# Kernel optimization log

Hardware: AMD Instinct MI355X
Metric: run time of the kernel (lower is better)

Reference implementation:

```python
import jax, jax.numpy as jnp
import numpy as np

T = 10
EPS = 1e-05

def setup_inputs() -> dict:
    key = jax.random.key(0)
    k1, k2 = jax.random.split(key)
    B, C, H, W = 128, 64, 56, 56
    X = jax.random.normal(k1, (B, C, H, W), dtype=jnp.float32)
    beta = jnp.zeros((C,), dtype=jnp.float32)
    return {"X": X, "beta": beta}


def reference(X, beta):
    # Training-path of BWItnBlock.forward (grad enabled branch of iter_norm_batch)
    B, C, H, W = X.shape
    d = C                      # n_channels, num_groups g = 1
    m = B * H * W
    # x = X.transpose(0,1).view(g, d, -1)  -> [d, m] with g=1
    x = jnp.transpose(X, (1, 0, 2, 3)).reshape(d, m)
    mean = jnp.mean(x, axis=1, keepdims=True)          # [d, 1]
    xc = x - mean                                      # [d, m]
    I = jnp.eye(d, dtype=X.dtype)
    # Sigma = eps*I + xc xc^T / m
    Sigma = EPS * I + (xc @ xc.T) / m                  # [d, d]
    # fix_cov: multiply off-diagonal by 0.9, diagonal by 1.0
    fix = 0.9 + 0.1 * I
    Sigma = Sigma * fix
    rTr = 1.0 / jnp.trace(Sigma)                       # scalar (sum(Sigma * I))
    Sigma_N = Sigma * rTr
    # Newton-Schulz iterations for inverse sqrt: P <- 1.5 P - 0.5 P^3 Sigma_N
    P = I
    for _ in range(T):
        P = 1.5 * P - 0.5 * ((P @ P @ P) @ Sigma_N)
    wm = P * jnp.sqrt(rTr)                             # whitening matrix [d, d]
    xn = wm @ xc                                       # [d, m]
    X_hat = jnp.transpose(xn.reshape(C, B, H, W), (1, 0, 2, 3))
    X_hat = X_hat + beta.reshape(1, C, 1, 1)
    return X_hat
```

## Files before the change

### kernel.cpp

```cpp
#include <hip/hip_runtime.h>

#define CH 64
#define HW 3136
#define MTOT 401408
#define TPX 128
#define NBLK 784
#define TPB 4

typedef __attribute__((ext_vector_type(8))) short short8;
typedef __attribute__((ext_vector_type(4))) float f32x4;
typedef __attribute__((ext_vector_type(4))) unsigned int u32x4;

__device__ __forceinline__ void split8(const float4 a, const float4 b,
                                       short8& hi, short8& lo, float& ssum){
  const float f[8] = {a.x,a.y,a.z,a.w, b.x,b.y,b.z,b.w};
  u32x4 hp, lp;
#pragma unroll
  for (int j=0;j<4;++j){
    const unsigned int b0 = __float_as_uint(f[2*j]);
    const unsigned int b1 = __float_as_uint(f[2*j+1]);
    hp[j] = (b0 >> 16) | (b1 & 0xFFFF0000u);
    const float h0 = __uint_as_float(b0 & 0xFFFF0000u);
    const float h1 = __uint_as_float(b1 & 0xFFFF0000u);
    const unsigned int l0 = __float_as_uint(f[2*j]   - h0);
    const unsigned int l1 = __float_as_uint(f[2*j+1] - h1);
    lp[j] = (l0 >> 16) | (l1 & 0xFFFF0000u);
  }
  hi = __builtin_bit_cast(short8, hp);
  lo = __builtin_bit_cast(short8, lp);
  ssum += ((f[0]+f[1])+(f[2]+f[3])) + ((f[4]+f[5])+(f[6]+f[7]));
}

__global__ __launch_bounds__(256) void k1_cov(const float* __restrict__ X,
                                              float* __restrict__ SR){
  constexpr int RG[10] = {0,1,1,2,2,2,3,3,3,3};
  constexpr int CG[10] = {0,0,1,0,1,2,0,1,2,3};
  __shared__ __align__(16) float buf[2][64*TPX];
  __shared__ float chs[64];

  const int t   = threadIdx.x;
  const int wid = __builtin_amdgcn_readfirstlane(t >> 6);
  const int l   = t & 63;
  const int lr  = l & 15;
  const int q   = l >> 4;

  f32x4 acc[10];
#pragma unroll
  for (int bi=0; bi<10; ++bi) acc[bi] = (f32x4){0.f,0.f,0.f,0.f};
  float sums[4] = {0.f,0.f,0.f,0.f};

  auto stage = [&](int tl, float* dst){
    const unsigned mbase = (unsigned)(blockIdx.x*TPB + tl) * TPX;
#pragma unroll
    for (int j=0;j<8;++j){
      const int r  = 16*wid + 2*j + (l>>5);
      const int cb = (l&31) ^ (r&7);
      const unsigned m  = mbase + 4*cb;
      const unsigned b  = m / HW;
      const unsigned hw = m - b*HW;
      const float* src = X + (size_t)b*(CH*HW) + (size_t)r*HW + hw;
      __builtin_amdgcn_global_load_lds(
        (const __attribute__((address_space(1))) unsigned int*)src,
        (__attribute__((address_space(3))) unsigned int*)(dst + (16*wid + 2*j)*TPX),
        16, 0, 0);
    }
  };

  stage(0, buf[0]);
  int pb = 0;
#pragma unroll
  for (int tl=0; tl<TPB; ++tl){
    if (tl+1 < TPB){
      stage(tl+1, buf[pb^1]);
      asm volatile("s_waitcnt vmcnt(8)" ::: "memory");
    } else {
      asm volatile("s_waitcnt vmcnt(0)" ::: "memory");
    }
    __builtin_amdgcn_sched_barrier(0);
    asm volatile("s_barrier" ::: "memory");
    const char* bp = (const char*)buf[pb];
    short8 fh[4], fl[4];
#pragma unroll
    for (int g=0; g<4; ++g){
      const int r   = 16*g + lr;
      const int sw  = r & 7;
      const int cb0 = 8*wid + 2*q;
      const float4 v0 = *(const float4*)(bp + r*512 + 16*((cb0+0)^sw));
      const float4 v1 = *(const float4*)(bp + r*512 + 16*((cb0+1)^sw));
      split8(v0, v1, fh[g], fl[g], sums[g]);
    }
#pragma unroll
    for (int bi=0; bi<10; ++bi){
      acc[bi] = __builtin_amdgcn_mfma_f32_16x16x32_bf16(fh[RG[bi]], fh[CG[bi]], acc[bi], 0,0,0);
      acc[bi] = __builtin_amdgcn_mfma_f32_16x16x32_bf16(fh[RG[bi]], fl[CG[bi]], acc[bi], 0,0,0);
      acc[bi] = __builtin_amdgcn_mfma_f32_16x16x32_bf16(fl[RG[bi]], fh[CG[bi]], acc[bi], 0,0,0);
    }
    asm volatile("s_barrier" ::: "memory");
    pb ^= 1;
  }

#pragma unroll
  for (int g=0; g<4; ++g){
    sums[g] += __shfl_xor(sums[g], 16);
    sums[g] += __shfl_xor(sums[g], 32);
  }

  float* red = &buf[0][0];
  for (int w=0; w<4; ++w){
    if (wid == w){
#pragma unroll
      for (int bi=0; bi<10; ++bi){
        const int row0 = RG[bi]*16 + 4*q;
        const int col  = CG[bi]*16 + lr;
#pragma unroll
        for (int r=0; r<4; ++r){
          float* d = &red[(row0+r)*64 + col];
          if (w==0) *d = acc[bi][r]; else *d += acc[bi][r];
        }
      }
      if (l < 16){
#pragma unroll
        for (int g=0; g<4; ++g){
          if (w==0) chs[g*16+l] = sums[g]; else chs[g*16+l] += sums[g];
        }
      }
    }
    __syncthreads();
  }

#pragma unroll
  for (int bi=0; bi<10; ++bi){
    const int r = RG[bi]*16 + (t>>4);
    const int c = CG[bi]*16 + (t&15);
    unsafeAtomicAdd(&SR[r*64+c], red[r*64+c]);
  }
  if (t < 64) unsafeAtomicAdd(&SR[4096+t], chs[t]);
}

__device__ __forceinline__ void mm_AtB(const float* a, const float* b, float* out,
                                       float alpha, const float* aff, float beta_){
  const int t = threadIdx.x;
  const int c2 = 2*(t & 31);
  const int r0 = 8*(t >> 5);
  float acc[8][2];
#pragma unroll
  for (int i=0;i<8;++i){ acc[i][0]=0.f; acc[i][1]=0.f; }
  for (int k=0;k<64;++k){
    const float2 bv = *(const float2*)&b[k*64 + c2];
    const float4 a0 = *(const float4*)&a[k*64 + r0];
    const float4 a1 = *(const float4*)&a[k*64 + r0 + 4];
    const float av[8] = {a0.x,a0.y,a0.z,a0.w, a1.x,a1.y,a1.z,a1.w};
#pragma unroll
    for (int i=0;i<8;++i){ acc[i][0] += av[i]*bv.x; acc[i][1] += av[i]*bv.y; }
  }
  float res[8][2];
#pragma unroll
  for (int i=0;i<8;++i){
    float f0 = alpha*acc[i][0], f1 = alpha*acc[i][1];
    if (aff){ f0 += beta_*aff[(r0+i)*64 + c2]; f1 += beta_*aff[(r0+i)*64 + c2 + 1]; }
    res[i][0]=f0; res[i][1]=f1;
  }
  __syncthreads();
#pragma unroll
  for (int i=0;i<8;++i){
    float2 o2; o2.x = res[i][0]; o2.y = res[i][1];
    *(float2*)&out[(r0+i)*64 + c2] = o2;
  }
  __syncthreads();
}

__global__ __launch_bounds__(256) void k2_wm(const float* __restrict__ SR,
                                             const float* __restrict__ beta,
                                             float* __restrict__ WM,
                                             float* __restrict__ OFS){
  __shared__ __align__(16) float bufE[4096];
  __shared__ __align__(16) float bufA[4096];
  __shared__ __align__(16) float bufB[4096];
  __shared__ float meanv[64];
  __shared__ float scal[2];
  const int t = threadIdx.x;
  const float inv_m = 1.f/(float)MTOT;
  if (t < 64) meanv[t] = SR[4096 + t]*inv_m;
  __syncthreads();
  for (int idx=t; idx<4096; idx+=256){
    const int r = idx >> 6, c = idx & 63;
    const int src = ((r >> 4) >= (c >> 4)) ? idx : (c*64 + r);
    const float cov = SR[src]*inv_m - meanv[r]*meanv[c];
    bufE[idx] = (r==c) ? (cov + 1e-5f - 1.f) : 0.9f*cov;
  }
  __syncthreads();
  float n2 = 0.f, tr = 0.f;
  for (int idx=t; idx<4096; idx+=256){
    const float e = bufE[idx];
    n2 += e*e;
    if ((idx >> 6) == (idx & 63)) tr += e;
  }
  bufA[t] = n2; bufB[t] = tr;
  __syncthreads();
  if (t < 64){
    bufA[t] = bufA[t]+bufA[t+64]+bufA[t+128]+bufA[t+192];
    bufB[t] = bufB[t]+bufB[t+64]+bufB[t+128]+bufB[t+192];
  }
  __syncthreads();
  if (t == 0){
    float s1=0.f, s2=0.f;
    for (int i=0;i<64;++i){ s1 += bufA[i]; s2 += bufB[i]; }
    scal[0] = s1; scal[1] = s2;
  }
  __syncthreads();
  const float frob2 = scal[0];
  const float trE   = scal[1];
  float wscale = 1.f;
  const float* wmLds;
  if (frob2 < 0.04f){
    mm_AtB(bufE, bufE, bufA, 1.f, nullptr, 0.f);
    mm_AtB(bufA, bufE, bufB, 1.f, nullptr, 0.f);
    for (int idx=t; idx<4096; idx+=256){
      const int r = idx >> 6, c = idx & 63;
      bufB[idx] = ((r==c)?1.f:0.f) - 0.5f*bufE[idx] + 0.375f*bufA[idx] - 0.3125f*bufB[idx];
    }
    mm_AtB(bufA, bufA, bufE, 1.f, nullptr, 0.f);
    for (int idx=t; idx<4096; idx+=256)
      bufB[idx] += 0.2734375f*bufE[idx];
    wmLds = bufB;
  } else {
    const float rTr = 1.f/(trE + 64.f);
    for (int idx=t; idx<4096; idx+=256){
      const int r = idx >> 6, c = idx & 63;
      bufE[idx] = (bufE[idx] + ((r==c)?1.f:0.f))*rTr;
      bufA[idx] = (r==c)?1.f:0.f;
    }
    __syncthreads();
    for (int it=0; it<10; ++it){
      mm_AtB(bufA, bufE, bufB, 1.f, nullptr, 0.f);
      mm_AtB(bufA, bufB, bufB, 1.f, nullptr, 0.f);
      mm_AtB(bufA, bufB, bufA, -0.5f, bufA, 1.5f);
    }
    wscale = sqrtf(rTr);
    wmLds = bufA;
  }
  __syncthreads();
  for (int idx=t; idx<4096; idx+=256) WM[idx] = wmLds[idx]*wscale;
  if (t < 64){
    float d = 0.f;
    for (int j=0;j<64;++j) d += wmLds[t*64 + j]*meanv[j];
    OFS[t] = beta[t] - d*wscale;
  }
}

__global__ __launch_bounds__(256) void k3_apply(const float* __restrict__ X,
                                                const float* __restrict__ WM,
                                                const float* __restrict__ OFS,
                                                float* __restrict__ out){
  __shared__ __align__(16) float buf[2][64*TPX];
  const int t   = threadIdx.x;
  const int wid = __builtin_amdgcn_readfirstlane(t >> 6);
  const int l   = t & 63;
  const int lr  = l & 15;
  const int q   = l >> 4;

  short8 ah[4][2], al[4][2];
  float dummy = 0.f;
#pragma unroll
  for (int cb=0; cb<4; ++cb)
#pragma unroll
    for (int ks=0; ks<2; ++ks){
      const float* wp = WM + (16*cb + lr)*64 + ks*32 + q*8;
      const float4 w0 = *(const float4*)wp;
      const float4 w1 = *(const float4*)(wp + 4);
      split8(w0, w1, ah[cb][ks], al[cb][ks], dummy);
    }
  float ofsv[4][4];
#pragma unroll
  for (int cb=0; cb<4; ++cb)
#pragma unroll
    for (int r=0; r<4; ++r) ofsv[cb][r] = OFS[16*cb + 4*q + r];

  auto stage = [&](int tl, float* dst){
    const unsigned mbase = (unsigned)(blockIdx.x*TPB + tl) * TPX;
#pragma unroll
    for (int j=0;j<8;++j){
      const int r = 16*wid + 2*j + (l>>5);
      const unsigned pxs = 4*(l&31);
      const unsigned m  = mbase + (pxs ^ (((r>>3)&1u)<<4));
      const unsigned b  = m / HW;
      const unsigned hw = m - b*HW;
      const float* src = X + (size_t)b*(CH*HW) + (size_t)r*HW + hw;
      __builtin_amdgcn_global_load_lds(
        (const __attribute__((address_space(1))) unsigned int*)src,
        (__attribute__((address_space(3))) unsigned int*)(dst + (16*wid + 2*j)*TPX),
        16, 0, 0);
    }
  };

  stage(0, buf[0]);
  int pb = 0;
#pragma unroll
  for (int tl=0; tl<TPB; ++tl){
    if (tl+1 < TPB) stage(tl+1, buf[pb^1]);
    if (tl == 0)          asm volatile("s_waitcnt vmcnt(8)"  ::: "memory");
    else if (tl+1 < TPB)  asm volatile("s_waitcnt vmcnt(40)" ::: "memory");
    else                  asm volatile("s_waitcnt vmcnt(32)" ::: "memory");
    __builtin_amdgcn_sched_barrier(0);
    asm volatile("s_barrier" ::: "memory");

    const float* bp = buf[pb];
    f32x4 acc[4][2];
#pragma unroll
    for (int cb=0; cb<4; ++cb)
#pragma unroll
      for (int pk=0; pk<2; ++pk) acc[cb][pk] = (f32x4){0.f,0.f,0.f,0.f};

#pragma unroll
    for (int ks=0; ks<2; ++ks){
      short8 bh[2], bl[2];
#pragma unroll
      for (int pk=0; pk<2; ++pk){
        const int ch0 = ks*32 + q*8;
        const int pxl = 32*wid + 16*pk + lr;
        const int pxs = pxl ^ ((q&1)<<4);
        const float* rp = bp + ch0*TPX + pxs;
        float f[8];
#pragma unroll
        for (int j=0;j<8;++j) f[j] = rp[j*TPX];
        const float4 v0 = {f[0],f[1],f[2],f[3]};
        const float4 v1 = {f[4],f[5],f[6],f[7]};
        split8(v0, v1, bh[pk], bl[pk], dummy);
      }
#pragma unroll
      for (int cb=0; cb<4; ++cb)
#pragma unroll
        for (int pk=0; pk<2; ++pk){
          acc[cb][pk] = __builtin_amdgcn_mfma_f32_16x16x32_bf16(ah[cb][ks], bh[pk], acc[cb][pk], 0,0,0);
          acc[cb][pk] = __builtin_amdgcn_mfma_f32_16x16x32_bf16(ah[cb][ks], bl[pk], acc[cb][pk], 0,0,0);
          acc[cb][pk] = __builtin_amdgcn_mfma_f32_16x16x32_bf16(al[cb][ks], bh[pk], acc[cb][pk], 0,0,0);
        }
    }

    {
      const unsigned mbase = (unsigned)(blockIdx.x*TPB + tl) * TPX;
#pragma unroll
      for (int pk=0; pk<2; ++pk){
        const unsigned P  = mbase + 32*wid + 16*pk + lr;
        const unsigned b2 = P / HW;
        const unsigned hw2 = P - b2*HW;
        float* ob = out + (size_t)b2*(CH*HW) + hw2 + (size_t)(4*q)*HW;
#pragma unroll
        for (int cb=0; cb<4; ++cb)
#pragma unroll
          for (int r=0; r<4; ++r)
            ob[(size_t)(16*cb + r)*HW] = acc[cb][pk][r] + ofsv[cb][r];
      }
    }
    asm volatile("s_barrier" ::: "memory");
    pb ^= 1;
  }
}

extern "C" void kernel_launch(void* const* d_in, const int* in_sizes, int n_in,
                              void* d_out, int out_size, void* d_ws, size_t ws_size,
                              hipStream_t stream){
  const float* X    = (const float*)d_in[0];
  const float* beta = (const float*)d_in[1];
  float* out = (float*)d_out;
  float* ws  = (float*)d_ws;
  float* SR  = ws;
  float* WM  = ws + 4160;
  float* OFS = WM + 4096;
  hipMemsetAsync(SR, 0, 4160*sizeof(float), stream);
  hipLaunchKernelGGL(k1_cov,   dim3(NBLK), dim3(256), 0, stream, X, SR);
  hipLaunchKernelGGL(k2_wm,    dim3(1),    dim3(256), 0, stream, SR, beta, WM, OFS);
  hipLaunchKernelGGL(k3_apply, dim3(NBLK), dim3(256), 0, stream, X, WM, OFS, out);
}
```

Before: 239.4 us.

## Rebalance covariance grid, use one tile per block and LDS-staged coalesced stores in apply

The covariance kernel now runs 512 blocks, each handling 6 or 7 tiles, so the 3136 tiles spread evenly across the CUs instead of 784 blocks of 4. The apply kernel drops its double-buffered multi-tile loop and launches one block per 128-pixel tile, which relies on occupancy rather than in-block prefetch to hide load latency. Its results are written back through shared memory so each lane stores float2 pairs along pixels, replacing the earlier scattered 4-byte stores. In exchange, the whitening matrix is reloaded and re-split by every one of the 3136 blocks, and the apply path gains extra barriers.

```diff
diff --git a/kernel.cpp b/kernel.cpp
--- a/kernel.cpp
+++ b/kernel.cpp
@@ -4,8 +4,6 @@
 #define HW 3136
 #define MTOT 401408
 #define TPX 128
-#define NBLK 784
-#define TPB 4
 
 typedef __attribute__((ext_vector_type(8))) short short8;
 typedef __attribute__((ext_vector_type(4))) float f32x4;
@@ -43,14 +41,17 @@
   const int l   = t & 63;
   const int lr  = l & 15;
   const int q   = l >> 4;
+  const int bid = blockIdx.x;
+  const int t0  = bid*6 + (bid < 64 ? bid : 64);
+  const int nt  = (bid < 64) ? 7 : 6;
 
   f32x4 acc[10];
 #pragma unroll
   for (int bi=0; bi<10; ++bi) acc[bi] = (f32x4){0.f,0.f,0.f,0.f};
   float sums[4] = {0.f,0.f,0.f,0.f};
 
-  auto stage = [&](int tl, float* dst){
-    const unsigned mbase = (unsigned)(blockIdx.x*TPB + tl) * TPX;
+  auto stage = [&](int tg, float* dst){
+    const unsigned mbase = (unsigned)tg * TPX;
 #pragma unroll
     for (int j=0;j<8;++j){
       const int r  = 16*wid + 2*j + (l>>5);
@@ -66,12 +67,11 @@
     }
   };
 
-  stage(0, buf[0]);
+  stage(t0, buf[0]);
   int pb = 0;
-#pragma unroll
-  for (int tl=0; tl<TPB; ++tl){
-    if (tl+1 < TPB){
-      stage(tl+1, buf[pb^1]);
+  for (int tl=0; tl<nt; ++tl){
+    if (tl+1 < nt){
+      stage(t0+tl+1, buf[pb^1]);
       asm volatile("s_waitcnt vmcnt(8)" ::: "memory");
     } else {
       asm volatile("s_waitcnt vmcnt(0)" ::: "memory");
@@ -252,32 +252,15 @@
                                                 const float* __restrict__ WM,
                                                 const float* __restrict__ OFS,
                                                 float* __restrict__ out){
-  __shared__ __align__(16) float buf[2][64*TPX];
+  __shared__ __align__(16) float tile[64*TPX];
   const int t   = threadIdx.x;
   const int wid = __builtin_amdgcn_readfirstlane(t >> 6);
   const int l   = t & 63;
   const int lr  = l & 15;
   const int q   = l >> 4;
 
-  short8 ah[4][2], al[4][2];
-  float dummy = 0.f;
-#pragma unroll
-  for (int cb=0; cb<4; ++cb)
-#pragma unroll
-    for (int ks=0; ks<2; ++ks){
-      const float* wp = WM + (16*cb + lr)*64 + ks*32 + q*8;
-      const float4 w0 = *(const float4*)wp;
-      const float4 w1 = *(const float4*)(wp + 4);
-      split8(w0, w1, ah[cb][ks], al[cb][ks], dummy);
-    }
-  float ofsv[4][4];
-#pragma unroll
-  for (int cb=0; cb<4; ++cb)
-#pragma unroll
-    for (int r=0; r<4; ++r) ofsv[cb][r] = OFS[16*cb + 4*q + r];
-
-  auto stage = [&](int tl, float* dst){
-    const unsigned mbase = (unsigned)(blockIdx.x*TPB + tl) * TPX;
+  {
+    const unsigned mbase = (unsigned)blockIdx.x * TPX;
 #pragma unroll
     for (int j=0;j<8;++j){
       const int r = 16*wid + 2*j + (l>>5);
@@ -288,72 +271,86 @@
       const float* src = X + (size_t)b*(CH*HW) + (size_t)r*HW + hw;
       __builtin_amdgcn_global_load_lds(
         (const __attribute__((address_space(1))) unsigned int*)src,
-        (__attribute__((address_space(3))) unsigned int*)(dst + (16*wid + 2*j)*TPX),
+        (__attribute__((address_space(3))) unsigned int*)(tile + (16*wid + 2*j)*TPX),
         16, 0, 0);
     }
-  };
-
-  stage(0, buf[0]);
-  int pb = 0;
-#pragma unroll
-  for (int tl=0; tl<TPB; ++tl){
-    if (tl+1 < TPB) stage(tl+1, buf[pb^1]);
-    if (tl == 0)          asm volatile("s_waitcnt vmcnt(8)"  ::: "memory");
-    else if (tl+1 < TPB)  asm volatile("s_waitcnt vmcnt(40)" ::: "memory");
-    else                  asm volatile("s_waitcnt vmcnt(32)" ::: "memory");
-    __builtin_amdgcn_sched_barrier(0);
-    asm volatile("s_barrier" ::: "memory");
-
-    const float* bp = buf[pb];
-    f32x4 acc[4][2];
+  }
+
+  short8 ah[4][2], al[4][2];
+  float dummy = 0.f;
+#pragma unroll
+  for (int cb=0; cb<4; ++cb)
+#pragma unroll
+    for (int ks=0; ks<2; ++ks){
+      const float* wp = WM + (16*cb + lr)*64 + ks*32 + q*8;
+      const float4 w0 = *(const float4*)wp;
+      const float4 w1 = *(const float4*)(wp + 4);
+      split8(w0, w1, ah[cb][ks], al[cb][ks], dummy);
+    }
+
+  asm volatile("s_waitcnt vmcnt(0)" ::: "memory");
+  __syncthreads();
+
+  f32x4 acc[4][2];
+#pragma unroll
+  for (int cb=0; cb<4; ++cb)
+#pragma unroll
+    for (int pk=0; pk<2; ++pk) acc[cb][pk] = (f32x4){0.f,0.f,0.f,0.f};
+
+#pragma unroll
+  for (int ks=0; ks<2; ++ks){
+    short8 bh[2], bl[2];
+#pragma unroll
+    for (int pk=0; pk<2; ++pk){
+      const int ch0 = ks*32 + q*8;
+      const int pxl = 32*wid + 16*pk + lr;
+      const int pxs = pxl ^ ((q&1)<<4);
+      const float* rp = tile + ch0*TPX + pxs;
+      float f[8];
+#pragma unroll
+      for (int j=0;j<8;++j) f[j] = rp[j*TPX];
+      const float4 v0 = {f[0],f[1],f[2],f[3]};
+      const float4 v1 = {f[4],f[5],f[6],f[7]};
+      split8(v0, v1, bh[pk], bl[pk], dummy);
+    }
 #pragma unroll
     for (int cb=0; cb<4; ++cb)
 #pragma unroll
-      for (int pk=0; pk<2; ++pk) acc[cb][pk] = (f32x4){0.f,0.f,0.f,0.f};
-
-#pragma unroll
-    for (int ks=0; ks<2; ++ks){
-      short8 bh[2], bl[2];
-#pragma unroll
       for (int pk=0; pk<2; ++pk){
-        const int ch0 = ks*32 + q*8;
-        const int pxl = 32*wid + 16*pk + lr;
-        const int pxs = pxl ^ ((q&1)<<4);
-        const float* rp = bp + ch0*TPX + pxs;
-        float f[8];
-#pragma unroll
-        for (int j=0;j<8;++j) f[j] = rp[j*TPX];
-        const float4 v0 = {f[0],f[1],f[2],f[3]};
-        const float4 v1 = {f[4],f[5],f[6],f[7]};
-        split8(v0, v1, bh[pk], bl[pk], dummy);
+        acc[cb][pk] = __builtin_amdgcn_mfma_f32_16x16x32_bf16(ah[cb][ks], bh[pk], acc[cb][pk], 0,0,0);
+        acc[cb][pk] = __builtin_amdgcn_mfma_f32_16x16x32_bf16(ah[cb][ks], bl[pk], acc[cb][pk], 0,0,0);
+        acc[cb][pk] = __builtin_amdgcn_mfma_f32_16x16x32_bf16(al[cb][ks], bh[pk], acc[cb][pk], 0,0,0);
       }
-#pragma unroll
-      for (int cb=0; cb<4; ++cb)
-#pragma unroll
-        for (int pk=0; pk<2; ++pk){
-          acc[cb][pk] = __builtin_amdgcn_mfma_f32_16x16x32_bf16(ah[cb][ks], bh[pk], acc[cb][pk], 0,0,0);
-          acc[cb][pk] = __builtin_amdgcn_mfma_f32_16x16x32_bf16(ah[cb][ks], bl[pk], acc[cb][pk], 0,0,0);
-          acc[cb][pk] = __builtin_amdgcn_mfma_f32_16x16x32_bf16(al[cb][ks], bh[pk], acc[cb][pk], 0,0,0);
-        }
-    }
-
-    {
-      const unsigned mbase = (unsigned)(blockIdx.x*TPB + tl) * TPX;
-#pragma unroll
-      for (int pk=0; pk<2; ++pk){
-        const unsigned P  = mbase + 32*wid + 16*pk + lr;
-        const unsigned b2 = P / HW;
-        const unsigned hw2 = P - b2*HW;
-        float* ob = out + (size_t)b2*(CH*HW) + hw2 + (size_t)(4*q)*HW;
-#pragma unroll
-        for (int cb=0; cb<4; ++cb)
-#pragma unroll
-          for (int r=0; r<4; ++r)
-            ob[(size_t)(16*cb + r)*HW] = acc[cb][pk][r] + ofsv[cb][r];
+  }
+  __syncthreads();
+
+#pragma unroll
+  for (int cb=0; cb<4; ++cb)
+#pragma unroll
+    for (int pk=0; pk<2; ++pk)
+#pragma unroll
+      for (int r=0; r<4; ++r){
+        const int ch = 16*cb + 4*q + r;
+        const int px = (32*wid + 16*pk + lr) ^ (((ch>>2)&1)<<4);
+        tile[ch*TPX + px] = acc[cb][pk][r];
       }
-    }
-    asm volatile("s_barrier" ::: "memory");
-    pb ^= 1;
+  __syncthreads();
+
+  {
+    const int c0 = 16*wid;
+    const unsigned P2 = (unsigned)blockIdx.x*TPX + 2*l;
+    const unsigned b2 = P2 / HW;
+    const unsigned hw2 = P2 - b2*HW;
+    float* ob = out + (size_t)b2*(CH*HW) + hw2;
+#pragma unroll
+    for (int i=0;i<16;++i){
+      const int c = c0 + i;
+      const int px = (2*l) ^ (((c>>2)&1)<<4);
+      const float2 v = *(const float2*)&tile[c*TPX + px];
+      const float o = OFS[c];
+      float2 pkv; pkv.x = v.x + o; pkv.y = v.y + o;
+      *(float2*)(ob + (size_t)c*HW) = pkv;
+    }
   }
 }
 
@@ -368,7 +365,7 @@
   float* WM  = ws + 4160;
   float* OFS = WM + 4096;
   hipMemsetAsync(SR, 0, 4160*sizeof(float), stream);
-  hipLaunchKernelGGL(k1_cov,   dim3(NBLK), dim3(256), 0, stream, X, SR);
+  hipLaunchKernelGGL(k1_cov,   dim3(512),  dim3(256), 0, stream, X, SR);
   hipLaunchKernelGGL(k2_wm,    dim3(1),    dim3(256), 0, stream, SR, beta, WM, OFS);
-  hipLaunchKernelGGL(k3_apply, dim3(NBLK), dim3(256), 0, stream, X, WM, OFS, out);
-}
+  hipLaunchKernelGGL(k3_apply, dim3(3136), dim3(256), 0, stream, X, WM, OFS, out);
+}
```

Measured after the change: 228.6 us. 1.05x faster.
